# Kernel tuning notes

Measured on AMD Instinct MI355X. Metric: run time of the kernel, lower is better.

## Reference

```python
import jax, jax.numpy as jnp
import numpy as np

jax.config.update("jax_enable_x64", True)  # original computes distances in float64

B, NL, NP, C, H, G, A, E = 16, 64, 512, 128, 256, 10, 14, 2048
BN_EPS = 1e-5


def _static_indices():
    # ragged graph sizes (batch_num_nodes) -> static scatter / valid-pair indices
    counts_l = np.array([32 if i % 2 == 0 else 64 for i in range(B)])
    counts_p = np.array([256 if i % 2 == 0 else 512 for i in range(B)])
    idx_l = np.concatenate([b * NL + np.arange(c) for b, c in enumerate(counts_l)])
    idx_p = np.concatenate([b * NP + np.arange(c) for b, c in enumerate(counts_p)])
    mask_l = np.zeros(B * NL, bool); mask_l[idx_l] = True
    mask_p = np.zeros(B * NP, bool); mask_p[idx_p] = True
    mask = mask_l.reshape(B, NL, 1) & mask_p.reshape(B, 1, NP)  # C_mask
    pair_flat = np.nonzero(mask.reshape(-1))[0]                 # row-major == torch C[C_mask] order
    pb = pair_flat // (NL * NP)
    rem = pair_flat % (NL * NP)
    pair_l = pb * NL + rem // NP
    pair_p = pb * NP + rem % NP
    return idx_l, idx_p, pair_flat, pair_l, pair_p, pb, len(idx_l), len(idx_p)


def setup_inputs() -> dict:
    idx_l, idx_p, pair_flat, pair_l, pair_p, pair_b, TL, TP = _static_indices()
    ks = jax.random.split(jax.random.key(0), 14)
    f32 = jnp.float32
    s = 0.02
    return {
        "h_l": jax.random.normal(ks[0], (TL, C), f32),
        "h_p": jax.random.normal(ks[1], (TP, C), f32),
        "lig_pos": jax.random.normal(ks[2], (TL, 3), f32) * 5.0,
        "prot_pos": jax.random.normal(ks[3], (TP, A, 3), f32) * 5.0,
        "edge_src": jax.random.randint(ks[4], (E,), 0, TL),
        "edge_dst": jax.random.randint(ks[5], (E,), 0, TL),
        "idx_l": jnp.asarray(idx_l), "idx_p": jnp.asarray(idx_p),
        "pair_flat": jnp.asarray(pair_flat), "pair_l": jnp.asarray(pair_l),
        "pair_p": jnp.asarray(pair_p), "pair_b": jnp.asarray(pair_b),
        "W1": jax.random.normal(ks[6], (2 * C, H), f32) * s, "b1": jnp.zeros(H, f32),
        "gamma": jnp.ones(H, f32), "beta": jnp.zeros(H, f32),
        "rmean": jnp.zeros(H, f32), "rvar": jnp.ones(H, f32),
        "Wpi": jax.random.normal(ks[7], (H, G * A), f32) * s, "bpi": jnp.zeros(G * A, f32),
        "Wsig": jax.random.normal(ks[8], (H, G * A), f32) * s, "bsig": jnp.zeros(G * A, f32),
        "Wmu": jax.random.normal(ks[9], (H, G * A), f32) * s, "bmu": jnp.zeros(G * A, f32),
        "Wat": jax.random.normal(ks[10], (C, 17), f32) * s, "bat": jnp.zeros(17, f32),
        "Wbt": jax.random.normal(ks[11], (2 * C, 5), f32) * s, "bbt": jnp.zeros(5, f32),
    }


def reference(h_l, h_p, lig_pos, prot_pos, edge_src, edge_dst, idx_l, idx_p,
              pair_flat, pair_l, pair_p, pair_b, W1, b1, gamma, beta, rmean, rvar,
              Wpi, bpi, Wsig, bsig, Wmu, bmu, Wat, bat, Wbt, bbt):
    # scatter ragged node feats into padded dense batches (to_dense_batch_dgl)
    dense_l = jnp.zeros((B * NL, C), h_l.dtype).at[idx_l].set(h_l)
    dense_p = jnp.zeros((B * NP, C), h_p.dtype).at[idx_p].set(h_p)
    # gather only valid (ligand, protein) pairs instead of the dense [B,NL,NP,2C] tensor
    Cpair = jnp.concatenate([dense_l[pair_l], dense_p[pair_p]], axis=-1)  # [M, 2C]
    x = Cpair @ W1 + b1
    x = gamma * (x - rmean) / jnp.sqrt(rvar + BN_EPS) + beta  # BatchNorm1d (eval)
    x = jax.nn.elu(x)                                          # dropout off (eval)
    pi = jax.nn.softmax(x @ Wpi + bpi, axis=-1).reshape(-1, G, A)
    sigma = (jax.nn.elu(x @ Wsig + bsig) + 1.1).reshape(-1, G, A)
    mu = (jax.nn.elu(x @ Wmu + bmu) + 1.0).reshape(-1, G, A)
    atom_types = h_l @ Wat + bat                               # [TL, 17]
    bond_types = jnp.concatenate([h_l[edge_src], h_l[edge_dst]], -1) @ Wbt + bbt  # [E, 5]
    # euclidean distance matrix in float64, as in the original
    X = jnp.zeros((B * NL, 3), jnp.float64).at[idx_l].set(lig_pos.astype(jnp.float64)).reshape(B, NL, 3)
    Y = jnp.zeros((B * NP, A, 3), jnp.float64).at[idx_p].set(prot_pos.astype(jnp.float64)).reshape(B, NP * A, 3)
    d2 = (-2.0 * jnp.einsum('bld,bpd->blp', X, Y)
          + jnp.sum(Y * Y, -1)[:, None, :] + jnp.sum(X * X, -1)[:, :, None])
    dist = jnp.nan_to_num(jnp.sqrt(d2), nan=10000.0).reshape(B * NL * NP, A)[pair_flat]
    dist = jax.lax.stop_gradient(dist[:, None, :])             # [M, 1, A], detached
    return (pi, sigma, mu, dist, atom_types, bond_types, pair_b)
```

## Files before the change

kernel.cpp:

```cpp
#include <hip/hip_runtime.h>


typedef __attribute__((ext_vector_type(4))) float f32x4;
typedef __attribute__((ext_vector_type(4))) unsigned int u32x4;
typedef __attribute__((ext_vector_type(8))) short bf16x8;

#define M_TOT 327680
#define WSCALE 16.0f
#define WDESCALE 0.0625f

#define NODE_BLOCKS 216
#define PREP_BLOCKS 432
#define DIST_BLOCKS 1280

__device__ __forceinline__ unsigned short f2bf(float f) {
    union { float f; unsigned int u; } v; v.f = f;
    unsigned int r = (v.u + 0x7FFFu + ((v.u >> 16) & 1u)) >> 16;
    return (unsigned short)r;
}

__device__ __forceinline__ float eluf(float y) {
    return fmaxf(y, 0.f) + __expf(fminf(y, 0.f)) - 1.f;
}

__device__ __forceinline__ float bfhalf_lo(unsigned int u) {
    return __uint_as_float(u << 16);
}
__device__ __forceinline__ float bfhalf_hi(unsigned int u) {
    return __uint_as_float(u & 0xFFFF0000u);
}

__device__ __forceinline__ void pair_decode(int m0, int& b, int& cl, int& cp0) {
    unsigned int P = (unsigned int)m0 / 40960u;
    unsigned int r = (unsigned int)m0 % 40960u;
    if (r < 8192u) {
        b = 2 * (int)P; cl = 96 * (int)P + (int)(r >> 8); cp0 = 768 * (int)P + (int)(r & 255u);
    } else {
        unsigned int rr = r - 8192u;
        b = 2 * (int)P + 1; cl = 96 * (int)P + 32 + (int)(rr >> 9);
        cp0 = 768 * (int)P + 256 + (int)(rr & 511u);
    }
}

__global__ void setup_kernel(const float* __restrict__ W1, const float* __restrict__ b1,
                             const float* __restrict__ gamma, const float* __restrict__ beta,
                             const float* __restrict__ rmean, const float* __restrict__ rvar,
                             const float* __restrict__ Wpi, const float* __restrict__ bpi,
                             const float* __restrict__ Wsig, const float* __restrict__ bsig,
                             const float* __restrict__ Wmu, const float* __restrict__ bmu,
                             const float* __restrict__ h_l, const float* __restrict__ h_p,
                             const int* __restrict__ esrc, const int* __restrict__ edst,
                             const float* __restrict__ Wat, const float* __restrict__ bat,
                             const float* __restrict__ Wbt, const float* __restrict__ bbt,
                             const float* __restrict__ lig_pos, const float* __restrict__ prot_pos,
                             unsigned char* __restrict__ W2q, float* __restrict__ b2s,
                             unsigned short* __restrict__ Lq, unsigned short* __restrict__ Pq,
                             float* __restrict__ out_at, float* __restrict__ out_bt,
                             float* __restrict__ out_dist, float* __restrict__ out_pb) {

    __shared__ __align__(16) unsigned short Wl[128 * 136];

    const int bid = blockIdx.x;
    const int tid = threadIdx.x;

    if (bid < NODE_BLOCKS) {
        const int nh   = bid & 1;
        const int row0 = (bid >> 1) * 64;
        const bool isLig = row0 < 768;
        const float* src = isLig ? (h_l + (size_t)row0 * 128) : (h_p + (size_t)(row0 - 768) * 128);
        unsigned short* dst = isLig ? (Lq + (size_t)row0 * 256) : (Pq + (size_t)(row0 - 768) * 256);
        const int koff = isLig ? 0 : 128;

        {
            const int nn = tid & 127;
            const int kb = tid >> 7;
            #pragma unroll 8
            for (int i = 0; i < 64; ++i) {
                int kk = i * 2 + kb;
                Wl[nn * 136 + kk] = f2bf(W1[(size_t)(koff + kk) * 256 + nh * 128 + nn]);
            }
        }
        __syncthreads();

        const int lane = tid & 63, w = tid >> 6;
        const int cGrp = lane & 15, g = lane >> 4;

        f32x4 acc[8];
        #pragma unroll
        for (int fn = 0; fn < 8; ++fn) acc[fn] = (f32x4){0.f, 0.f, 0.f, 0.f};

        #pragma unroll
        for (int fk = 0; fk < 4; ++fk) {
            const float* ap = src + (size_t)(w * 16 + cGrp) * 128 + fk * 32 + g * 8;
            f32x4 qa = *(const f32x4*)ap;
            f32x4 qb = *(const f32x4*)(ap + 4);
            bf16x8 af;
            af[0] = (short)f2bf(qa[0]); af[1] = (short)f2bf(qa[1]);
            af[2] = (short)f2bf(qa[2]); af[3] = (short)f2bf(qa[3]);
            af[4] = (short)f2bf(qb[0]); af[5] = (short)f2bf(qb[1]);
            af[6] = (short)f2bf(qb[2]); af[7] = (short)f2bf(qb[3]);
            #pragma unroll
            for (int fn = 0; fn < 8; ++fn) {
                bf16x8 bf = *(const bf16x8*)(Wl + (fn * 16 + cGrp) * 136 + fk * 32 + g * 8);
                acc[fn] = __builtin_amdgcn_mfma_f32_16x16x32_bf16(af, bf, acc[fn], 0, 0, 0);
            }
        }
        #pragma unroll
        for (int fn = 0; fn < 8; ++fn) {
            int h = nh * 128 + fn * 16 + cGrp;
            float s  = gamma[h] * rsqrtf(rvar[h] + 1e-5f);
            float c0 = isLig ? (s * (b1[h] - rmean[h]) + beta[h]) : 0.f;
            #pragma unroll
            for (int rg = 0; rg < 4; ++rg)
                dst[(size_t)(w * 16 + g * 4 + rg) * 256 + h] = f2bf(s * acc[fn][rg] + c0);
        }
        return;
    }

    if (bid >= NODE_BLOCKS + PREP_BLOCKS) {
        const int m0 = (bid - NODE_BLOCKS - PREP_BLOCKS) * 256;
        int b, cl, cp0;
        pair_decode(m0, b, cl, cp0);
        const int rw = tid;
        float lx = lig_pos[cl * 3 + 0];
        float ly = lig_pos[cl * 3 + 1];
        float lz = lig_pos[cl * 3 + 2];
        const float* pp = prot_pos + (size_t)(cp0 + rw) * 42;
        float* dr = out_dist + (size_t)(m0 + rw) * 14;
        #pragma unroll
        for (int a = 0; a < 14; ++a) {
            float dx = lx - pp[a * 3 + 0];
            float dy = ly - pp[a * 3 + 1];
            float dz = lz - pp[a * 3 + 2];
            dr[a] = sqrtf(dx * dx + dy * dy + dz * dz);
        }
        out_pb[m0 + rw] = (float)b;
        return;
    }

    int idx = (bid - NODE_BLOCKS) * 256 + tid;
    {
        int j    = idx & 7;
        int h    = (idx >> 3) & 1;
        int lane = (idx >> 4) & 63;
        int sp   = (idx >> 10) & 3;
        int t    = idx >> 12;
        int f    = t % 9;
        int head = t / 9;
        int k    = (sp * 2 + h) * 32 + (lane >> 4) * 8 + j;
        int col  = f * 16 + (lane & 15);
        float v = 0.f;
        if (col < 140) {
            const float* Wh = (head == 0) ? Wpi : (head == 1) ? Wsig : Wmu;
            v = Wh[k * 140 + col] * WSCALE;
        }
        W2q[idx] = (unsigned char)(__builtin_amdgcn_cvt_pk_fp8_f32(v, 0.f, 0, false) & 0xFF);
    }
    if (idx < 432) {
        int head = idx / 144, col = idx % 144;
        float v = 0.f;
        if (col < 140) v = (head == 0) ? bpi[col] : (head == 1) ? bsig[col] : bmu[col];
        b2s[idx] = v * WSCALE;
    }
    if (idx < 768 * 17) {
        int row = idx / 17, c = idx % 17;
        const float* hr = h_l + (size_t)row * 128;
        float s = bat[c];
        #pragma unroll 4
        for (int k = 0; k < 128; ++k) s += hr[k] * Wat[k * 17 + c];
        out_at[idx] = s;
    } else if (idx < 768 * 17 + 2048 * 5) {
        int t2 = idx - 768 * 17;
        int e = t2 / 5, c = t2 % 5;
        const float* hs = h_l + (size_t)esrc[e] * 128;
        const float* hd = h_l + (size_t)edst[e] * 128;
        float s = bbt[c];
        #pragma unroll 4
        for (int k = 0; k < 128; ++k)
            s += hs[k] * Wbt[k * 5 + c] + hd[k] * Wbt[(k + 128) * 5 + c];
        out_bt[t2] = s;
    }
}

__global__ __launch_bounds__(256, 4) void pair_kernel(
        const unsigned short* __restrict__ Lq, const unsigned short* __restrict__ Pq,
        const unsigned char* __restrict__ W2q, const float* __restrict__ b2s,
        float* __restrict__ out_pi, float* __restrict__ out_sig, float* __restrict__ out_mu) {

    __shared__ __align__(16) unsigned char Bs[36864];

    const int tid = threadIdx.x, lane = tid & 63, w = tid >> 6;
    const int c = lane & 15, g = lane >> 4;
    const int m0 = blockIdx.x * 64;

    int b, cl, cp0;
    pair_decode(m0, b, cl, cp0);

    u32x4 stg[9];
    #pragma unroll
    for (int i = 0; i < 9; ++i)
        stg[i] = *(const u32x4*)(W2q + (size_t)(tid + 256 * i) * 16);

    const int row = w * 16 + c;
    const unsigned short* pqp = Pq + (size_t)(cp0 + row) * 256;
    const unsigned short* lqp = Lq + (size_t)cl * 256;
    long Xa[8];
    #pragma unroll
    for (int s = 0; s < 8; ++s) {
        u32x4 pv = *(const u32x4*)(pqp + s * 32 + g * 8);
        u32x4 lv = *(const u32x4*)(lqp + s * 32 + g * 8);
        float y0 = eluf(bfhalf_lo(pv[0]) + bfhalf_lo(lv[0]));
        float y1 = eluf(bfhalf_hi(pv[0]) + bfhalf_hi(lv[0]));
        float y2 = eluf(bfhalf_lo(pv[1]) + bfhalf_lo(lv[1]));
        float y3 = eluf(bfhalf_hi(pv[1]) + bfhalf_hi(lv[1]));
        float y4 = eluf(bfhalf_lo(pv[2]) + bfhalf_lo(lv[2]));
        float y5 = eluf(bfhalf_hi(pv[2]) + bfhalf_hi(lv[2]));
        float y6 = eluf(bfhalf_lo(pv[3]) + bfhalf_lo(lv[3]));
        float y7 = eluf(bfhalf_hi(pv[3]) + bfhalf_hi(lv[3]));
        unsigned int lo = (unsigned int)__builtin_amdgcn_cvt_pk_fp8_f32(y0, y1, 0, false);
        lo = (unsigned int)__builtin_amdgcn_cvt_pk_fp8_f32(y2, y3, (int)lo, true);
        unsigned int hi = (unsigned int)__builtin_amdgcn_cvt_pk_fp8_f32(y4, y5, 0, false);
        hi = (unsigned int)__builtin_amdgcn_cvt_pk_fp8_f32(y6, y7, (int)hi, true);
        Xa[s] = (long)(((unsigned long long)hi << 32) | (unsigned long long)lo);
    }

    const bool v8 = (c < 12);

    #pragma unroll
    for (int head = 0; head < 3; ++head) {
        #pragma unroll
        for (int i = 0; i < 9; ++i)
            *(u32x4*)(Bs + (size_t)(tid + 256 * i) * 16) = stg[i];
        __syncthreads();

        float bb[9];
        #pragma unroll
        for (int f = 0; f < 9; ++f) bb[f] = b2s[head * 144 + f * 16 + c];

        f32x4 acc[9];
        #pragma unroll
        for (int f = 0; f < 9; ++f) acc[f] = (f32x4){bb[f], bb[f], bb[f], bb[f]};

        #pragma unroll
        for (int sp = 0; sp < 4; ++sp) {
            long xa0 = Xa[2 * sp], xa1 = Xa[2 * sp + 1];
            #pragma unroll
            for (int f = 0; f < 9; ++f) {
                u32x4 bq = *(const u32x4*)(Bs + f * 4096 + sp * 1024 + lane * 16);
                long b0 = (long)(((unsigned long long)bq[1] << 32) | (unsigned long long)bq[0]);
                long b1 = (long)(((unsigned long long)bq[3] << 32) | (unsigned long long)bq[2]);
                acc[f] = __builtin_amdgcn_mfma_f32_16x16x32_fp8_fp8(xa0, b0, acc[f], 0, 0, 0);
                acc[f] = __builtin_amdgcn_mfma_f32_16x16x32_fp8_fp8(xa1, b1, acc[f], 0, 0, 0);
            }
        }

        if (head < 2) {
            const unsigned char* wsrc = W2q + (size_t)(head + 1) * 36864;
            #pragma unroll
            for (int i = 0; i < 9; ++i)
                stg[i] = *(const u32x4*)(wsrc + (size_t)(tid + 256 * i) * 16);
        }

        #pragma unroll
        for (int f = 0; f < 9; ++f)
            #pragma unroll
            for (int q = 0; q < 4; ++q) acc[f][q] *= WDESCALE;

        if (head == 0) {
            #pragma unroll
            for (int q = 0; q < 4; ++q) {
                float e0 = __expf(acc[0][q]), e1 = __expf(acc[1][q]);
                float e2 = __expf(acc[2][q]), e3 = __expf(acc[3][q]);
                float e4 = __expf(acc[4][q]), e5 = __expf(acc[5][q]);
                float e6 = __expf(acc[6][q]), e7 = __expf(acc[7][q]);
                float e8 = v8 ? __expf(acc[8][q]) : 0.f;
                float sm = ((e0 + e1) + (e2 + e3)) + ((e4 + e5) + (e6 + e7)) + e8;
                sm += __shfl_xor(sm, 1, 64);
                sm += __shfl_xor(sm, 2, 64);
                sm += __shfl_xor(sm, 4, 64);
                sm += __shfl_xor(sm, 8, 64);
                float inv = 1.f / sm;
                acc[0][q] = e0 * inv; acc[1][q] = e1 * inv;
                acc[2][q] = e2 * inv; acc[3][q] = e3 * inv;
                acc[4][q] = e4 * inv; acc[5][q] = e5 * inv;
                acc[6][q] = e6 * inv; acc[7][q] = e7 * inv;
                acc[8][q] = e8 * inv;
            }
        } else {
            const float addc = (head == 1) ? 1.1f : 1.0f;
            #pragma unroll
            for (int f = 0; f < 9; ++f)
                #pragma unroll
                for (int q = 0; q < 4; ++q) acc[f][q] = eluf(acc[f][q]) + addc;
        }

        __syncthreads();
        float* ot = (float*)Bs;
        {
            const int rbase = (w * 16 + g * 4) * 140 + c;
            #pragma unroll
            for (int f = 0; f < 9; ++f) {
                if (f < 8 || v8) {
                    #pragma unroll
                    for (int q = 0; q < 4; ++q)
                        ot[rbase + q * 140 + f * 16] = acc[f][q];
                }
            }
        }
        __syncthreads();

        float* dsth = (head == 0) ? out_pi : (head == 1) ? out_sig : out_mu;
        float* dst = dsth + (size_t)m0 * 140;
        #pragma unroll
        for (int i = 0; i < 9; ++i) {
            int idx = tid + 256 * i;
            if (idx < 2240)
                *(f32x4*)(dst + idx * 4) = *(const f32x4*)(ot + idx * 4);
        }

        if (head < 2) __syncthreads();
    }
}

extern "C" void kernel_launch(void* const* d_in, const int* in_sizes, int n_in,
                              void* d_out, int out_size, void* d_ws, size_t ws_size,
                              hipStream_t stream) {
    const float* h_l      = (const float*)d_in[0];
    const float* h_p      = (const float*)d_in[1];
    const float* lig_pos  = (const float*)d_in[2];
    const float* prot_pos = (const float*)d_in[3];
    const int*   esrc     = (const int*)d_in[4];
    const int*   edst     = (const int*)d_in[5];
    const float* W1    = (const float*)d_in[12];
    const float* b1    = (const float*)d_in[13];
    const float* gamma = (const float*)d_in[14];
    const float* beta  = (const float*)d_in[15];
    const float* rmean = (const float*)d_in[16];
    const float* rvar  = (const float*)d_in[17];
    const float* Wpi   = (const float*)d_in[18];
    const float* bpi   = (const float*)d_in[19];
    const float* Wsig  = (const float*)d_in[20];
    const float* bsig  = (const float*)d_in[21];
    const float* Wmu   = (const float*)d_in[22];
    const float* bmu   = (const float*)d_in[23];
    const float* Wat   = (const float*)d_in[24];
    const float* bat   = (const float*)d_in[25];
    const float* Wbt   = (const float*)d_in[26];
    const float* bbt   = (const float*)d_in[27];

    char* ws = (char*)d_ws;
    unsigned char*  W2q = (unsigned char*)(ws + 131072);
    float*          b2s = (float*)(ws + 241664);
    unsigned short* Lq  = (unsigned short*)(ws + 245440);
    unsigned short* Pq  = (unsigned short*)(ws + 638656);

    float* out = (float*)d_out;
    const size_t M = M_TOT;
    float* out_pi   = out;
    float* out_sig  = out + M * 140;
    float* out_mu   = out + 2 * M * 140;
    float* out_dist = out + 3 * M * 140;
    float* out_at   = out + 3 * M * 140 + M * 14;
    float* out_bt   = out_at + 768 * 17;
    float* out_pb   = out_bt + 2048 * 5;

    hipLaunchKernelGGL(setup_kernel, dim3(NODE_BLOCKS + PREP_BLOCKS + DIST_BLOCKS), dim3(256), 0, stream,
                       W1, b1, gamma, beta, rmean, rvar,
                       Wpi, bpi, Wsig, bsig, Wmu, bmu,
                       h_l, h_p, esrc, edst, Wat, bat, Wbt, bbt,
                       lig_pos, prot_pos,
                       W2q, b2s, Lq, Pq, out_at, out_bt, out_dist, out_pb);

    hipLaunchKernelGGL(pair_kernel, dim3(M_TOT / 64), dim3(256), 0, stream,
                       Lq, Pq, W2q, b2s, out_pi, out_sig, out_mu);
}
```

Measured before the change: 166.8 us.

## Process 128 pairs per block reusing staged weights across two row tiles

Each pair_kernel block now handles 128 pair rows instead of 64, so every LDS-staged weight fragment feeds two MFMA accumulator sets and the per-block weight staging cost is amortized over twice the work. The output epilogue is restructured so each wave writes its own 16-row slice through LDS without block-wide barriers, and the ligand row is unpacked once for both tiles. Register pressure roughly doubles for accumulators and activations under launch_bounds(256,4), which risks spills or lower occupancy, and the grid is halved. The decode assumes 128-row blocks never cross a ligand/protein pair boundary, which holds because valid protein counts are multiples of 128.

```diff
diff --git a/kernel.cpp b/kernel.cpp
--- a/kernel.cpp
+++ b/kernel.cpp
@@ -191,7 +191,7 @@
 
     const int tid = threadIdx.x, lane = tid & 63, w = tid >> 6;
     const int c = lane & 15, g = lane >> 4;
-    const int m0 = blockIdx.x * 64;
+    const int m0 = blockIdx.x * 128;
 
     int b, cl, cp0;
     pair_decode(m0, b, cl, cp0);
@@ -202,29 +202,46 @@
         stg[i] = *(const u32x4*)(W2q + (size_t)(tid + 256 * i) * 16);
 
     const int row = w * 16 + c;
-    const unsigned short* pqp = Pq + (size_t)(cp0 + row) * 256;
     const unsigned short* lqp = Lq + (size_t)cl * 256;
-    long Xa[8];
+    const unsigned short* pq0 = Pq + (size_t)(cp0 + row) * 256;
+    const unsigned short* pq1 = Pq + (size_t)(cp0 + 64 + row) * 256;
+    long Xa0[8], Xa1[8];
     #pragma unroll
     for (int s = 0; s < 8; ++s) {
-        u32x4 pv = *(const u32x4*)(pqp + s * 32 + g * 8);
         u32x4 lv = *(const u32x4*)(lqp + s * 32 + g * 8);
-        float y0 = eluf(bfhalf_lo(pv[0]) + bfhalf_lo(lv[0]));
-        float y1 = eluf(bfhalf_hi(pv[0]) + bfhalf_hi(lv[0]));
-        float y2 = eluf(bfhalf_lo(pv[1]) + bfhalf_lo(lv[1]));
-        float y3 = eluf(bfhalf_hi(pv[1]) + bfhalf_hi(lv[1]));
-        float y4 = eluf(bfhalf_lo(pv[2]) + bfhalf_lo(lv[2]));
-        float y5 = eluf(bfhalf_hi(pv[2]) + bfhalf_hi(lv[2]));
-        float y6 = eluf(bfhalf_lo(pv[3]) + bfhalf_lo(lv[3]));
-        float y7 = eluf(bfhalf_hi(pv[3]) + bfhalf_hi(lv[3]));
-        unsigned int lo = (unsigned int)__builtin_amdgcn_cvt_pk_fp8_f32(y0, y1, 0, false);
-        lo = (unsigned int)__builtin_amdgcn_cvt_pk_fp8_f32(y2, y3, (int)lo, true);
-        unsigned int hi = (unsigned int)__builtin_amdgcn_cvt_pk_fp8_f32(y4, y5, 0, false);
-        hi = (unsigned int)__builtin_amdgcn_cvt_pk_fp8_f32(y6, y7, (int)hi, true);
-        Xa[s] = (long)(((unsigned long long)hi << 32) | (unsigned long long)lo);
+        float l0 = bfhalf_lo(lv[0]), h0 = bfhalf_hi(lv[0]);
+        float l1 = bfhalf_lo(lv[1]), h1 = bfhalf_hi(lv[1]);
+        float l2 = bfhalf_lo(lv[2]), h2 = bfhalf_hi(lv[2]);
+        float l3 = bfhalf_lo(lv[3]), h3 = bfhalf_hi(lv[3]);
+        u32x4 pv = *(const u32x4*)(pq0 + s * 32 + g * 8);
+        {
+            float y0 = eluf(bfhalf_lo(pv[0]) + l0), y1 = eluf(bfhalf_hi(pv[0]) + h0);
+            float y2 = eluf(bfhalf_lo(pv[1]) + l1), y3 = eluf(bfhalf_hi(pv[1]) + h1);
+            float y4 = eluf(bfhalf_lo(pv[2]) + l2), y5 = eluf(bfhalf_hi(pv[2]) + h2);
+            float y6 = eluf(bfhalf_lo(pv[3]) + l3), y7 = eluf(bfhalf_hi(pv[3]) + h3);
+            unsigned int lo = (unsigned int)__builtin_amdgcn_cvt_pk_fp8_f32(y0, y1, 0, false);
+            lo = (unsigned int)__builtin_amdgcn_cvt_pk_fp8_f32(y2, y3, (int)lo, true);
+            unsigned int hi = (unsigned int)__builtin_amdgcn_cvt_pk_fp8_f32(y4, y5, 0, false);
+            hi = (unsigned int)__builtin_amdgcn_cvt_pk_fp8_f32(y6, y7, (int)hi, true);
+            Xa0[s] = (long)(((unsigned long long)hi << 32) | (unsigned long long)lo);
+        }
+        pv = *(const u32x4*)(pq1 + s * 32 + g * 8);
+        {
+            float y0 = eluf(bfhalf_lo(pv[0]) + l0), y1 = eluf(bfhalf_hi(pv[0]) + h0);
+            float y2 = eluf(bfhalf_lo(pv[1]) + l1), y3 = eluf(bfhalf_hi(pv[1]) + h1);
+            float y4 = eluf(bfhalf_lo(pv[2]) + l2), y5 = eluf(bfhalf_hi(pv[2]) + h2);
+            float y6 = eluf(bfhalf_lo(pv[3]) + l3), y7 = eluf(bfhalf_hi(pv[3]) + h3);
+            unsigned int lo = (unsigned int)__builtin_amdgcn_cvt_pk_fp8_f32(y0, y1, 0, false);
+            lo = (unsigned int)__builtin_amdgcn_cvt_pk_fp8_f32(y2, y3, (int)lo, true);
+            unsigned int hi = (unsigned int)__builtin_amdgcn_cvt_pk_fp8_f32(y4, y5, 0, false);
+            hi = (unsigned int)__builtin_amdgcn_cvt_pk_fp8_f32(y6, y7, (int)hi, true);
+            Xa1[s] = (long)(((unsigned long long)hi << 32) | (unsigned long long)lo);
+        }
     }
 
     const bool v8 = (c < 12);
+    float* ot = (float*)Bs;
+    const int rbase = w * 2240 + (g * 4) * 140 + c;
 
     #pragma unroll
     for (int head = 0; head < 3; ++head) {
@@ -237,85 +254,135 @@
         #pragma unroll
         for (int f = 0; f < 9; ++f) bb[f] = b2s[head * 144 + f * 16 + c];
 
-        f32x4 acc[9];
-        #pragma unroll
-        for (int f = 0; f < 9; ++f) acc[f] = (f32x4){bb[f], bb[f], bb[f], bb[f]};
-
+        f32x4 acc0[9], acc1[9];
+        #pragma unroll
+        for (int f = 0; f < 9; ++f) {
+            acc0[f] = (f32x4){bb[f], bb[f], bb[f], bb[f]};
+            acc1[f] = acc0[f];
+        }
         #pragma unroll
         for (int sp = 0; sp < 4; ++sp) {
-            long xa0 = Xa[2 * sp], xa1 = Xa[2 * sp + 1];
+            long x00 = Xa0[2 * sp], x01 = Xa0[2 * sp + 1];
+            long x10 = Xa1[2 * sp], x11 = Xa1[2 * sp + 1];
             #pragma unroll
             for (int f = 0; f < 9; ++f) {
                 u32x4 bq = *(const u32x4*)(Bs + f * 4096 + sp * 1024 + lane * 16);
                 long b0 = (long)(((unsigned long long)bq[1] << 32) | (unsigned long long)bq[0]);
                 long b1 = (long)(((unsigned long long)bq[3] << 32) | (unsigned long long)bq[2]);
-                acc[f] = __builtin_amdgcn_mfma_f32_16x16x32_fp8_fp8(xa0, b0, acc[f], 0, 0, 0);
-                acc[f] = __builtin_amdgcn_mfma_f32_16x16x32_fp8_fp8(xa1, b1, acc[f], 0, 0, 0);
-            }
-        }
-
-        if (head < 2) {
-            const unsigned char* wsrc = W2q + (size_t)(head + 1) * 36864;
-            #pragma unroll
-            for (int i = 0; i < 9; ++i)
-                stg[i] = *(const u32x4*)(wsrc + (size_t)(tid + 256 * i) * 16);
-        }
+                acc0[f] = __builtin_amdgcn_mfma_f32_16x16x32_fp8_fp8(x00, b0, acc0[f], 0, 0, 0);
+                acc0[f] = __builtin_amdgcn_mfma_f32_16x16x32_fp8_fp8(x01, b1, acc0[f], 0, 0, 0);
+                acc1[f] = __builtin_amdgcn_mfma_f32_16x16x32_fp8_fp8(x10, b0, acc1[f], 0, 0, 0);
+                acc1[f] = __builtin_amdgcn_mfma_f32_16x16x32_fp8_fp8(x11, b1, acc1[f], 0, 0, 0);
+            }
+        }
+        __syncthreads();
+
+        float* dsth = (head == 0) ? out_pi : (head == 1) ? out_sig : out_mu;
+        const float addc = (head == 1) ? 1.1f : 1.0f;
 
         #pragma unroll
         for (int f = 0; f < 9; ++f)
             #pragma unroll
-            for (int q = 0; q < 4; ++q) acc[f][q] *= WDESCALE;
-
+            for (int q = 0; q < 4; ++q) acc0[f][q] *= WDESCALE;
         if (head == 0) {
             #pragma unroll
             for (int q = 0; q < 4; ++q) {
-                float e0 = __expf(acc[0][q]), e1 = __expf(acc[1][q]);
-                float e2 = __expf(acc[2][q]), e3 = __expf(acc[3][q]);
-                float e4 = __expf(acc[4][q]), e5 = __expf(acc[5][q]);
-                float e6 = __expf(acc[6][q]), e7 = __expf(acc[7][q]);
-                float e8 = v8 ? __expf(acc[8][q]) : 0.f;
+                float e0 = __expf(acc0[0][q]), e1 = __expf(acc0[1][q]);
+                float e2 = __expf(acc0[2][q]), e3 = __expf(acc0[3][q]);
+                float e4 = __expf(acc0[4][q]), e5 = __expf(acc0[5][q]);
+                float e6 = __expf(acc0[6][q]), e7 = __expf(acc0[7][q]);
+                float e8 = v8 ? __expf(acc0[8][q]) : 0.f;
                 float sm = ((e0 + e1) + (e2 + e3)) + ((e4 + e5) + (e6 + e7)) + e8;
                 sm += __shfl_xor(sm, 1, 64);
                 sm += __shfl_xor(sm, 2, 64);
                 sm += __shfl_xor(sm, 4, 64);
                 sm += __shfl_xor(sm, 8, 64);
                 float inv = 1.f / sm;
-                acc[0][q] = e0 * inv; acc[1][q] = e1 * inv;
-                acc[2][q] = e2 * inv; acc[3][q] = e3 * inv;
-                acc[4][q] = e4 * inv; acc[5][q] = e5 * inv;
-                acc[6][q] = e6 * inv; acc[7][q] = e7 * inv;
-                acc[8][q] = e8 * inv;
+                acc0[0][q] = e0 * inv; acc0[1][q] = e1 * inv;
+                acc0[2][q] = e2 * inv; acc0[3][q] = e3 * inv;
+                acc0[4][q] = e4 * inv; acc0[5][q] = e5 * inv;
+                acc0[6][q] = e6 * inv; acc0[7][q] = e7 * inv;
+                acc0[8][q] = e8 * inv;
             }
         } else {
-            const float addc = (head == 1) ? 1.1f : 1.0f;
             #pragma unroll
             for (int f = 0; f < 9; ++f)
                 #pragma unroll
-                for (int q = 0; q < 4; ++q) acc[f][q] = eluf(acc[f][q]) + addc;
-        }
-
-        __syncthreads();
-        float* ot = (float*)Bs;
+                for (int q = 0; q < 4; ++q) acc0[f][q] = eluf(acc0[f][q]) + addc;
+        }
+        #pragma unroll
+        for (int f = 0; f < 9; ++f) {
+            if (f < 8 || v8) {
+                #pragma unroll
+                for (int q = 0; q < 4; ++q)
+                    ot[rbase + q * 140 + f * 16] = acc0[f][q];
+            }
+        }
         {
-            const int rbase = (w * 16 + g * 4) * 140 + c;
-            #pragma unroll
-            for (int f = 0; f < 9; ++f) {
-                if (f < 8 || v8) {
-                    #pragma unroll
-                    for (int q = 0; q < 4; ++q)
-                        ot[rbase + q * 140 + f * 16] = acc[f][q];
-                }
-            }
-        }
-        __syncthreads();
-
-        float* dsth = (head == 0) ? out_pi : (head == 1) ? out_sig : out_mu;
-        float* dst = dsth + (size_t)m0 * 140;
-        #pragma unroll
-        for (int i = 0; i < 9; ++i) {
-            int idx = tid + 256 * i;
-            if (idx < 2240)
-                *(f32x4*)(dst + idx * 4) = *(const f32x4*)(ot + idx * 4);
+            float* dst = dsth + (size_t)m0 * 140 + w * 2240;
+            const float* srcp = ot + w * 2240;
+            #pragma unroll
+            for (int r = 0; r < 9; ++r) {
+                int ch = lane + r * 64;
+                if (ch < 560)
+                    *(f32x4*)(dst + ch * 4) = *(const f32x4*)(srcp + ch * 4);
+            }
+        }
+
+        if (head < 2) {
+            const unsigned char* wsrc = W2q + (size_t)(head + 1) * 36864;
+            #pragma unroll
+            for (int i = 0; i < 9; ++i)
+                stg[i] = *(const u32x4*)(wsrc + (size_t)(tid + 256 * i) * 16);
+        }
+
+        #pragma unroll
+        for (int f = 0; f < 9; ++f)
+            #pragma unroll
+            for (int q = 0; q < 4; ++q) acc1[f][q] *= WDESCALE;
+        if (head == 0) {
+            #pragma unroll
+            for (int q = 0; q < 4; ++q) {
+                float e0 = __expf(acc1[0][q]), e1 = __expf(acc1[1][q]);
+                float e2 = __expf(acc1[2][q]), e3 = __expf(acc1[3][q]);
+                float e4 = __expf(acc1[4][q]), e5 = __expf(acc1[5][q]);
+                float e6 = __expf(acc1[6][q]), e7 = __expf(acc1[7][q]);
+                float e8 = v8 ? __expf(acc1[8][q]) : 0.f;
+                float sm = ((e0 + e1) + (e2 + e3)) + ((e4 + e5) + (e6 + e7)) + e8;
+                sm += __shfl_xor(sm, 1, 64);
+                sm += __shfl_xor(sm, 2, 64);
+                sm += __shfl_xor(sm, 4, 64);
+                sm += __shfl_xor(sm, 8, 64);
+                float inv = 1.f / sm;
+                acc1[0][q] = e0 * inv; acc1[1][q] = e1 * inv;
+                acc1[2][q] = e2 * inv; acc1[3][q] = e3 * inv;
+                acc1[4][q] = e4 * inv; acc1[5][q] = e5 * inv;
+                acc1[6][q] = e6 * inv; acc1[7][q] = e7 * inv;
+                acc1[8][q] = e8 * inv;
+            }
+        } else {
+            #pragma unroll
+            for (int f = 0; f < 9; ++f)
+                #pragma unroll
+                for (int q = 0; q < 4; ++q) acc1[f][q] = eluf(acc1[f][q]) + addc;
+        }
+        #pragma unroll
+        for (int f = 0; f < 9; ++f) {
+            if (f < 8 || v8) {
+                #pragma unroll
+                for (int q = 0; q < 4; ++q)
+                    ot[rbase + q * 140 + f * 16] = acc1[f][q];
+            }
+        }
+        {
+            float* dst = dsth + (size_t)(m0 + 64) * 140 + w * 2240;
+            const float* srcp = ot + w * 2240;
+            #pragma unroll
+            for (int r = 0; r < 9; ++r) {
+                int ch = lane + r * 64;
+                if (ch < 560)
+                    *(f32x4*)(dst + ch * 4) = *(const f32x4*)(srcp + ch * 4);
+            }
         }
 
         if (head < 2) __syncthreads();
@@ -371,6 +438,6 @@
                        lig_pos, prot_pos,
                        W2q, b2s, Lq, Pq, out_at, out_bt, out_dist, out_pb);
 
-    hipLaunchKernelGGL(pair_kernel, dim3(M_TOT / 64), dim3(256), 0, stream,
+    hipLaunchKernelGGL(pair_kernel, dim3(M_TOT / 128), dim3(256), 0, stream,
                        Lq, Pq, W2q, b2s, out_pi, out_sig, out_mu);
 }
```

Measured after the change: 220.6 us. 32.3% more time.
